# Performance work log

Hardware: AMD Instinct MI355X
Metric: run time of the kernel (lower is better)

Reference implementation:

```python
import jax, jax.numpy as jnp
import numpy as np

N_NODES = 50000
N_EDGES = 800000
D = 128


def setup_inputs() -> dict:
    key = jax.random.key(0)
    k1, k2, k3, k4 = jax.random.split(key, 4)
    feat = jax.random.normal(k1, (N_NODES, D), dtype=jnp.float32)
    W = jax.random.normal(k2, (D, D), dtype=jnp.float32) * (1.0 / np.sqrt(D))
    b = jnp.zeros((D,), dtype=jnp.float32)
    eps = jnp.zeros((1,), dtype=jnp.float32)
    src = jax.random.randint(k3, (N_EDGES,), 0, N_NODES, dtype=jnp.int64 if jax.config.jax_enable_x64 else jnp.int32)
    dst = jax.random.randint(k4, (N_EDGES,), 0, N_NODES, dtype=jnp.int64 if jax.config.jax_enable_x64 else jnp.int32)
    return {"feat": feat, "W": W, "b": b, "eps": eps, "src": src, "dst": dst}


def reference(feat, W, b, eps, src, dst):
    # message passing: m_e = feat[src_e]; neigh_i = sum_{e: dst_e = i} m_e
    msgs = feat[src]  # [E, D] gather
    neigh = jax.ops.segment_sum(msgs, dst, num_segments=N_NODES)  # [N, D]
    # eps-weighted residual: (1 + eps) * h_dst + neigh
    rst = (1.0 + eps) * feat + neigh  # eps is [1], broadcasts
    # apply_func: Dense(D)
    out = jnp.einsum('nd,de->ne', rst, W) + b
    return out
```

## Files before the change

kernel.cpp:

```cpp
#include <hip/hip_runtime.h>

#define D 128
#define CAP 32
#define OCAP 4096

typedef __attribute__((ext_vector_type(8))) short bf16x8;
typedef __attribute__((ext_vector_type(4))) float f32x4;

static __device__ inline short f2bf(float f) {
  union { float f; unsigned u; } v; v.f = f;
  unsigned r = v.u + 0x7FFF + ((v.u >> 16) & 1);
  return (short)(r >> 16);
}
static __device__ inline float bf_lo(unsigned u) {
  union { unsigned u; float f; } v; v.u = u << 16; return v.f;
}
static __device__ inline float bf_hi(unsigned u) {
  union { unsigned u; float f; } v; v.u = u & 0xFFFF0000u; return v.f;
}

static __device__ inline void wfrag_build_one(const float* __restrict__ W,
                                              uint4* __restrict__ wfrag, int t) {
  int c = t >> 8, h = (t >> 6) & 3, l = t & 63;
  int col = c * 16 + (l & 15);
  int k0 = h * 32 + (l >> 4) * 8;
  unsigned u[4];
  #pragma unroll
  for (int p = 0; p < 4; ++p) {
    unsigned lo = (unsigned short)f2bf(W[(k0 + 2 * p) * D + col]);
    unsigned hi = (unsigned short)f2bf(W[(k0 + 2 * p + 1) * D + col]);
    u[p] = lo | (hi << 16);
  }
  wfrag[t] = make_uint4(u[0], u[1], u[2], u[3]);
}

__global__ __launch_bounds__(256) void build_kernel(
    const int* __restrict__ src, const int* __restrict__ dst,
    int* __restrict__ cnt, int* __restrict__ ocount, unsigned* __restrict__ oflow,
    unsigned short* __restrict__ permfix,
    const float* __restrict__ W, uint4* __restrict__ wfrag,
    const float* __restrict__ feat, uint4* __restrict__ featbf,
    int E, int ND8) {
  int i = blockIdx.x * 256 + threadIdx.x;
  if (i < E) {
    int d = dst[i];
    int s = src[i];
    int c = atomicAdd(&cnt[d], 1);
    if (c < CAP) {
      permfix[(size_t)d * CAP + c] = (unsigned short)s;
    } else {
      int o = atomicAdd(ocount, 1);
      if (o < OCAP) oflow[o] = ((unsigned)d << 16) | (unsigned)s;
    }
  }
  if (i < ND8) {
    float4 u = ((const float4*)feat)[2 * i];
    float4 v = ((const float4*)feat)[2 * i + 1];
    unsigned w0 = (unsigned short)f2bf(u.x) | ((unsigned)(unsigned short)f2bf(u.y) << 16);
    unsigned w1 = (unsigned short)f2bf(u.z) | ((unsigned)(unsigned short)f2bf(u.w) << 16);
    unsigned w2 = (unsigned short)f2bf(v.x) | ((unsigned)(unsigned short)f2bf(v.y) << 16);
    unsigned w3 = (unsigned short)f2bf(v.z) | ((unsigned)(unsigned short)f2bf(v.w) << 16);
    featbf[i] = make_uint4(w0, w1, w2, w3);
  }
  if (i < 2048) wfrag_build_one(W, wfrag, i);
}

__global__ __launch_bounds__(256, 4) void fused_gather_gemm(
    const uint2* __restrict__ featbf, const float* __restrict__ eps,
    const float* __restrict__ bias, const int* __restrict__ cnt,
    const int* __restrict__ ocount, const unsigned* __restrict__ oflow,
    const unsigned short* __restrict__ permfix,
    const uint4* __restrict__ wfrag, float* __restrict__ out, int N) {
  __shared__ float xs[64][132];
  __shared__ float sbias[128];
  int tid = threadIdx.x;
  int base = blockIdx.x * 64;
  if (tid < 128) sbias[tid] = bias[tid];
  float scale = 1.0f + eps[0];

  int g = tid >> 5, lane = tid & 31;
  for (int it = 0; it < 8; ++it) {
    int lr = it * 8 + g;
    int grow = base + lr;
    float4 acc = make_float4(0.f, 0.f, 0.f, 0.f);
    if (grow < N) {
      uint2 a0 = featbf[(size_t)grow * 32 + lane];
      acc.x = scale * bf_lo(a0.x);
      acc.y = scale * bf_hi(a0.x);
      acc.z = scale * bf_lo(a0.y);
      acc.w = scale * bf_hi(a0.y);
      int deg = cnt[grow];
      deg = (deg < CAP) ? deg : CAP;
      const unsigned short* pf = permfix + (size_t)grow * CAP;
      int j = 0;
      for (; j + 8 <= deg; j += 8) {
        uint4 pv = *(const uint4*)&pf[j];
        int s0 = pv.x & 0xFFFF, s1 = pv.x >> 16;
        int s2 = pv.y & 0xFFFF, s3 = pv.y >> 16;
        int s4 = pv.z & 0xFFFF, s5 = pv.z >> 16;
        int s6 = pv.w & 0xFFFF, s7 = pv.w >> 16;
        uint2 r0 = featbf[(size_t)s0 * 32 + lane];
        uint2 r1 = featbf[(size_t)s1 * 32 + lane];
        uint2 r2 = featbf[(size_t)s2 * 32 + lane];
        uint2 r3 = featbf[(size_t)s3 * 32 + lane];
        uint2 r4 = featbf[(size_t)s4 * 32 + lane];
        uint2 r5 = featbf[(size_t)s5 * 32 + lane];
        uint2 r6 = featbf[(size_t)s6 * 32 + lane];
        uint2 r7 = featbf[(size_t)s7 * 32 + lane];
        acc.x += bf_lo(r0.x) + bf_lo(r1.x) + bf_lo(r2.x) + bf_lo(r3.x)
               + bf_lo(r4.x) + bf_lo(r5.x) + bf_lo(r6.x) + bf_lo(r7.x);
        acc.y += bf_hi(r0.x) + bf_hi(r1.x) + bf_hi(r2.x) + bf_hi(r3.x)
               + bf_hi(r4.x) + bf_hi(r5.x) + bf_hi(r6.x) + bf_hi(r7.x);
        acc.z += bf_lo(r0.y) + bf_lo(r1.y) + bf_lo(r2.y) + bf_lo(r3.y)
               + bf_lo(r4.y) + bf_lo(r5.y) + bf_lo(r6.y) + bf_lo(r7.y);
        acc.w += bf_hi(r0.y) + bf_hi(r1.y) + bf_hi(r2.y) + bf_hi(r3.y)
               + bf_hi(r4.y) + bf_hi(r5.y) + bf_hi(r6.y) + bf_hi(r7.y);
      }
      for (; j < deg; ++j) {
        uint2 a = featbf[(size_t)pf[j] * 32 + lane];
        acc.x += bf_lo(a.x); acc.y += bf_hi(a.x);
        acc.z += bf_lo(a.y); acc.w += bf_hi(a.y);
      }
    }
    *(float4*)&xs[lr][lane * 4] = acc;
  }
  __syncthreads();

  int novf = *ocount;
  novf = (novf < OCAP) ? novf : OCAP;
  if (novf > 0) {
    if (tid < 32) {
      for (int o = 0; o < novf; ++o) {
        unsigned e = oflow[o];
        int d = (int)(e >> 16);
        if ((d >> 6) == (int)blockIdx.x) {
          int s = (int)(e & 0xFFFF);
          uint2 a = featbf[(size_t)s * 32 + tid];
          int r = d & 63;
          xs[r][tid * 4 + 0] += bf_lo(a.x);
          xs[r][tid * 4 + 1] += bf_hi(a.x);
          xs[r][tid * 4 + 2] += bf_lo(a.y);
          xs[r][tid * 4 + 3] += bf_hi(a.y);
        }
      }
    }
    __syncthreads();
  }

  int w = tid >> 6;
  int l = tid & 63;
  int rowg = l >> 4, rl = l & 15;

  bf16x8 a[4];
  #pragma unroll
  for (int h = 0; h < 4; ++h) {
    const float* p = &xs[16 * w + rl][h * 32 + rowg * 8];
    float4 u = *(const float4*)p;
    float4 v = *(const float4*)(p + 4);
    bf16x8 t;
    t[0] = f2bf(u.x); t[1] = f2bf(u.y); t[2] = f2bf(u.z); t[3] = f2bf(u.w);
    t[4] = f2bf(v.x); t[5] = f2bf(v.y); t[6] = f2bf(v.z); t[7] = f2bf(v.w);
    a[h] = t;
  }

  const bf16x8* wf = (const bf16x8*)wfrag;
  #pragma unroll
  for (int c = 0; c < 8; ++c) {
    float bb = sbias[c * 16 + rl];
    f32x4 acc = {bb, bb, bb, bb};
    #pragma unroll
    for (int h = 0; h < 4; ++h) {
      bf16x8 b = wf[(c * 4 + h) * 64 + l];
      acc = __builtin_amdgcn_mfma_f32_16x16x32_bf16(a[h], b, acc, 0, 0, 0);
    }
    #pragma unroll
    for (int r = 0; r < 4; ++r) {
      int row = base + 16 * w + rowg * 4 + r;
      if (row < N) out[(size_t)row * D + c * 16 + rl] = acc[r];
    }
  }
}

__global__ __launch_bounds__(256) void init_out_kernel(
    const float* __restrict__ feat, const float* __restrict__ eps,
    float* __restrict__ out, int n4) {
  int i = blockIdx.x * blockDim.x + threadIdx.x;
  if (i >= n4) return;
  float scale = 1.0f + eps[0];
  float4 v = ((const float4*)feat)[i];
  v.x *= scale; v.y *= scale; v.z *= scale; v.w *= scale;
  ((float4*)out)[i] = v;
}

__global__ __launch_bounds__(256) void scatter_add_kernel(
    const float* __restrict__ feat, const int* __restrict__ src,
    const int* __restrict__ dst, float* __restrict__ out, int E) {
  int gid = blockIdx.x * blockDim.x + threadIdx.x;
  int e = gid >> 5;
  int lane = gid & 31;
  if (e >= E) return;
  int s = src[e], d = dst[e];
  float4 v = ((const float4*)(feat + (size_t)s * D))[lane];
  float* o = out + (size_t)d * D + lane * 4;
  unsafeAtomicAdd(o + 0, v.x);
  unsafeAtomicAdd(o + 1, v.y);
  unsafeAtomicAdd(o + 2, v.z);
  unsafeAtomicAdd(o + 3, v.w);
}

#define ROWS 64
__global__ __launch_bounds__(256) void gemm_inplace_kernel(
    float* __restrict__ out, const float* __restrict__ Wm,
    const float* __restrict__ bias, int N) {
  __shared__ float Ws[D * D];
  __shared__ float xs[ROWS * D];
  int tid = threadIdx.x;
  int base = blockIdx.x * ROWS;
  #pragma unroll
  for (int it = 0; it < 16; ++it) {
    int idx = tid + 256 * it;
    ((float4*)Ws)[idx] = ((const float4*)Wm)[idx];
  }
  #pragma unroll
  for (int it = 0; it < 8; ++it) {
    int idx = tid + 256 * it;
    int row = idx >> 5, c4 = idx & 31;
    float4 v = make_float4(0.f, 0.f, 0.f, 0.f);
    if (base + row < N) v = ((const float4*)(out + (size_t)(base + row) * D))[c4];
    ((float4*)xs)[row * 32 + c4] = v;
  }
  __syncthreads();
  int tc = tid & 31, tr = tid >> 5;
  float acc[8][4];
  #pragma unroll
  for (int r = 0; r < 8; ++r)
    #pragma unroll
    for (int i = 0; i < 4; ++i) acc[r][i] = 0.f;
  for (int k0 = 0; k0 < D; k0 += 4) {
    float4 f[8];
    #pragma unroll
    for (int r = 0; r < 8; ++r) f[r] = *(const float4*)&xs[(tr * 8 + r) * D + k0];
    float w[4][4];
    #pragma unroll
    for (int u = 0; u < 4; ++u)
      #pragma unroll
      for (int i = 0; i < 4; ++i) w[u][i] = Ws[(k0 + u) * D + tc + 32 * i];
    #pragma unroll
    for (int r = 0; r < 8; ++r)
      #pragma unroll
      for (int i = 0; i < 4; ++i) {
        acc[r][i] += f[r].x * w[0][i];
        acc[r][i] += f[r].y * w[1][i];
        acc[r][i] += f[r].z * w[2][i];
        acc[r][i] += f[r].w * w[3][i];
      }
  }
  float bv[4];
  #pragma unroll
  for (int i = 0; i < 4; ++i) bv[i] = bias[tc + 32 * i];
  #pragma unroll
  for (int r = 0; r < 8; ++r) {
    int row = base + tr * 8 + r;
    if (row < N) {
      #pragma unroll
      for (int i = 0; i < 4; ++i)
        out[(size_t)row * D + tc + 32 * i] = acc[r][i] + bv[i];
    }
  }
}

extern "C" void kernel_launch(void* const* d_in, const int* in_sizes, int n_in,
                              void* d_out, int out_size, void* d_ws, size_t ws_size,
                              hipStream_t stream) {
  const float* feat = (const float*)d_in[0];
  const float* Wm   = (const float*)d_in[1];
  const float* bias = (const float*)d_in[2];
  const float* eps  = (const float*)d_in[3];
  const int*   src  = (const int*)d_in[4];
  const int*   dst  = (const int*)d_in[5];
  float* out = (float*)d_out;

  int N = in_sizes[0] / D;
  int E = in_sizes[4];
  int ND8 = (N * D) / 8;

  size_t cnt_b    = (size_t)N * 4;
  size_t ocount_b = 4;
  size_t oflow_b  = (size_t)OCAP * 4;
  size_t perm_b   = (size_t)N * CAP * 2;
  size_t wfrag_off = (cnt_b + ocount_b + oflow_b + perm_b + 15) & ~(size_t)15;
  size_t featbf_off = wfrag_off + 2048 * 16;
  size_t needed = featbf_off + (size_t)N * D * 2;

  if (ws_size >= needed) {
    int* cnt = (int*)d_ws;
    int* ocount = cnt + N;
    unsigned* oflow = (unsigned*)(ocount + 1);
    unsigned short* permfix = (unsigned short*)(oflow + OCAP);
    uint4* wfrag = (uint4*)((char*)d_ws + wfrag_off);
    uint4* featbf = (uint4*)((char*)d_ws + featbf_off);

    hipMemsetAsync(cnt, 0, cnt_b + ocount_b, stream);

    int gmax = max(E, ND8);
    build_kernel<<<(gmax + 255) / 256, 256, 0, stream>>>(
        src, dst, cnt, ocount, oflow, permfix, Wm, wfrag, feat, featbf, E, ND8);

    fused_gather_gemm<<<(N + 63) / 64, 256, 0, stream>>>(
        (const uint2*)featbf, eps, bias, cnt, ocount, oflow, permfix, wfrag, out, N);
  } else {
    int n4 = (N * D) / 4;
    init_out_kernel<<<(n4 + 255) / 256, 256, 0, stream>>>(feat, eps, out, n4);
    long long total_threads = (long long)E * 32;
    int sblocks = (int)((total_threads + 255) / 256);
    scatter_add_kernel<<<sblocks, 256, 0, stream>>>(feat, src, dst, out, E);
    int gblocks2 = (N + ROWS - 1) / ROWS;
    gemm_inplace_kernel<<<gblocks2, 256, 0, stream>>>(out, Wm, bias, N);
  }
}
```

Measured before the change: 114.1 us.

## Shrink gather-GEMM tile to 32 rows, vectorize edge build, add 4-wide tail

The build kernel now has each thread read four edges at once with int4 loads and insert them one after another, which cuts the build grid to a quarter of its edge-sized width. The fused gather+GEMM kernel uses 32-row tiles instead of 64, which doubles the block count and raises the occupancy hint to 8 blocks per CU. The four waves are remapped so each computes a 16-row by 64-column MFMA output quadrant. A 4-edge unrolled step is added before the scalar tail of the neighbour gather to give the tail more memory-level parallelism. The trade-off is a longer serial chain of atomics per build thread and a repeated overflow scan in twice as many blocks.

```diff
diff --git a/kernel.cpp b/kernel.cpp
--- a/kernel.cpp
+++ b/kernel.cpp
@@ -3,6 +3,7 @@
 #define D 128
 #define CAP 32
 #define OCAP 4096
+#define TILE 32
 
 typedef __attribute__((ext_vector_type(8))) short bf16x8;
 typedef __attribute__((ext_vector_type(4))) float f32x4;
@@ -32,6 +33,18 @@
     u[p] = lo | (hi << 16);
   }
   wfrag[t] = make_uint4(u[0], u[1], u[2], u[3]);
+}
+
+static __device__ inline void edge_insert(
+    int s, int d, int* __restrict__ cnt, int* __restrict__ ocount,
+    unsigned* __restrict__ oflow, unsigned short* __restrict__ permfix) {
+  int c = atomicAdd(&cnt[d], 1);
+  if (c < CAP) {
+    permfix[(size_t)d * CAP + c] = (unsigned short)s;
+  } else {
+    int o = atomicAdd(ocount, 1);
+    if (o < OCAP) oflow[o] = ((unsigned)d << 16) | (unsigned)s;
+  }
 }
 
 __global__ __launch_bounds__(256) void build_kernel(
@@ -42,16 +55,17 @@
     const float* __restrict__ feat, uint4* __restrict__ featbf,
     int E, int ND8) {
   int i = blockIdx.x * 256 + threadIdx.x;
-  if (i < E) {
-    int d = dst[i];
-    int s = src[i];
-    int c = atomicAdd(&cnt[d], 1);
-    if (c < CAP) {
-      permfix[(size_t)d * CAP + c] = (unsigned short)s;
-    } else {
-      int o = atomicAdd(ocount, 1);
-      if (o < OCAP) oflow[o] = ((unsigned)d << 16) | (unsigned)s;
-    }
+  int e0 = i * 4;
+  if (e0 + 4 <= E) {
+    int4 s4 = *(const int4*)&src[e0];
+    int4 d4 = *(const int4*)&dst[e0];
+    edge_insert(s4.x, d4.x, cnt, ocount, oflow, permfix);
+    edge_insert(s4.y, d4.y, cnt, ocount, oflow, permfix);
+    edge_insert(s4.z, d4.z, cnt, ocount, oflow, permfix);
+    edge_insert(s4.w, d4.w, cnt, ocount, oflow, permfix);
+  } else if (e0 < E) {
+    for (int e = e0; e < E; ++e)
+      edge_insert(src[e], dst[e], cnt, ocount, oflow, permfix);
   }
   if (i < ND8) {
     float4 u = ((const float4*)feat)[2 * i];
@@ -65,21 +79,21 @@
   if (i < 2048) wfrag_build_one(W, wfrag, i);
 }
 
-__global__ __launch_bounds__(256, 4) void fused_gather_gemm(
+__global__ __launch_bounds__(256, 8) void fused_gather_gemm(
     const uint2* __restrict__ featbf, const float* __restrict__ eps,
     const float* __restrict__ bias, const int* __restrict__ cnt,
     const int* __restrict__ ocount, const unsigned* __restrict__ oflow,
     const unsigned short* __restrict__ permfix,
     const uint4* __restrict__ wfrag, float* __restrict__ out, int N) {
-  __shared__ float xs[64][132];
+  __shared__ float xs[TILE][132];
   __shared__ float sbias[128];
   int tid = threadIdx.x;
-  int base = blockIdx.x * 64;
+  int base = blockIdx.x * TILE;
   if (tid < 128) sbias[tid] = bias[tid];
   float scale = 1.0f + eps[0];
 
   int g = tid >> 5, lane = tid & 31;
-  for (int it = 0; it < 8; ++it) {
+  for (int it = 0; it < TILE / 8; ++it) {
     int lr = it * 8 + g;
     int grow = base + lr;
     float4 acc = make_float4(0.f, 0.f, 0.f, 0.f);
@@ -116,6 +130,20 @@
         acc.w += bf_hi(r0.y) + bf_hi(r1.y) + bf_hi(r2.y) + bf_hi(r3.y)
                + bf_hi(r4.y) + bf_hi(r5.y) + bf_hi(r6.y) + bf_hi(r7.y);
       }
+      if (j + 4 <= deg) {
+        uint2 pv = *(const uint2*)&pf[j];
+        int s0 = pv.x & 0xFFFF, s1 = pv.x >> 16;
+        int s2 = pv.y & 0xFFFF, s3 = pv.y >> 16;
+        uint2 r0 = featbf[(size_t)s0 * 32 + lane];
+        uint2 r1 = featbf[(size_t)s1 * 32 + lane];
+        uint2 r2 = featbf[(size_t)s2 * 32 + lane];
+        uint2 r3 = featbf[(size_t)s3 * 32 + lane];
+        acc.x += bf_lo(r0.x) + bf_lo(r1.x) + bf_lo(r2.x) + bf_lo(r3.x);
+        acc.y += bf_hi(r0.x) + bf_hi(r1.x) + bf_hi(r2.x) + bf_hi(r3.x);
+        acc.z += bf_lo(r0.y) + bf_lo(r1.y) + bf_lo(r2.y) + bf_lo(r3.y);
+        acc.w += bf_hi(r0.y) + bf_hi(r1.y) + bf_hi(r2.y) + bf_hi(r3.y);
+        j += 4;
+      }
       for (; j < deg; ++j) {
         uint2 a = featbf[(size_t)pf[j] * 32 + lane];
         acc.x += bf_lo(a.x); acc.y += bf_hi(a.x);
@@ -133,10 +161,10 @@
       for (int o = 0; o < novf; ++o) {
         unsigned e = oflow[o];
         int d = (int)(e >> 16);
-        if ((d >> 6) == (int)blockIdx.x) {
+        if ((d / TILE) == (int)blockIdx.x) {
           int s = (int)(e & 0xFFFF);
           uint2 a = featbf[(size_t)s * 32 + tid];
-          int r = d & 63;
+          int r = d % TILE;
           xs[r][tid * 4 + 0] += bf_lo(a.x);
           xs[r][tid * 4 + 1] += bf_hi(a.x);
           xs[r][tid * 4 + 2] += bf_lo(a.y);
@@ -150,11 +178,13 @@
   int w = tid >> 6;
   int l = tid & 63;
   int rowg = l >> 4, rl = l & 15;
+  int rs = (w & 1) * 16;
+  int cb = (w >> 1) * 4;
 
   bf16x8 a[4];
   #pragma unroll
   for (int h = 0; h < 4; ++h) {
-    const float* p = &xs[16 * w + rl][h * 32 + rowg * 8];
+    const float* p = &xs[rs + rl][h * 32 + rowg * 8];
     float4 u = *(const float4*)p;
     float4 v = *(const float4*)(p + 4);
     bf16x8 t;
@@ -165,7 +195,8 @@
 
   const bf16x8* wf = (const bf16x8*)wfrag;
   #pragma unroll
-  for (int c = 0; c < 8; ++c) {
+  for (int cl = 0; cl < 4; ++cl) {
+    int c = cb + cl;
     float bb = sbias[c * 16 + rl];
     f32x4 acc = {bb, bb, bb, bb};
     #pragma unroll
@@ -175,7 +206,7 @@
     }
     #pragma unroll
     for (int r = 0; r < 4; ++r) {
-      int row = base + 16 * w + rowg * 4 + r;
+      int row = base + rs + rowg * 4 + r;
       if (row < N) out[(size_t)row * D + c * 16 + rl] = acc[r];
     }
   }
@@ -302,11 +333,11 @@
 
     hipMemsetAsync(cnt, 0, cnt_b + ocount_b, stream);
 
-    int gmax = max(E, ND8);
+    int gmax = max((E + 3) / 4, ND8);
     build_kernel<<<(gmax + 255) / 256, 256, 0, stream>>>(
         src, dst, cnt, ocount, oflow, permfix, Wm, wfrag, feat, featbf, E, ND8);
 
-    fused_gather_gemm<<<(N + 63) / 64, 256, 0, stream>>>(
+    fused_gather_gemm<<<(N + TILE - 1) / TILE, 256, 0, stream>>>(
         (const uint2*)featbf, eps, bias, cnt, ocount, oflow, permfix, wfrag, out, N);
   } else {
     int n4 = (N * D) / 4;
```

Result: faster. 111.6 us (-2.2%).
